# Optimization experiments

Hardware: AMD Instinct MI355X
Metric: run time of the kernel (lower is better)

The kernel has to match this reference:

```python
import jax, jax.numpy as jnp
import numpy as np

DIM = 1024
N_HEADS = 16
HEAD_DIM = DIM // N_HEADS
B, T = 2, 2048


def setup_inputs() -> dict:
    key = jax.random.key(0)
    kx, kq, kk, kv, ko = jax.random.split(key, 5)
    x = jax.random.normal(kx, (B, T, DIM), dtype=jnp.float32)
    # additive causal mask: 0 on/below diagonal, -inf above
    neg = jnp.finfo(jnp.float32).min
    causal = jnp.triu(jnp.full((T, T), neg, dtype=jnp.float32), k=1)
    mask = causal[None, None, :, :]  # [1,1,T,T]
    scale = 0.02
    Wq = jax.random.normal(kq, (DIM, DIM), dtype=jnp.float32) * scale
    Wk = jax.random.normal(kk, (DIM, DIM), dtype=jnp.float32) * scale
    Wv = jax.random.normal(kv, (DIM, DIM), dtype=jnp.float32) * scale
    Wo = jax.random.normal(ko, (DIM, DIM), dtype=jnp.float32) * scale
    return {"x": x, "mask": mask, "Wq": Wq, "Wk": Wk, "Wv": Wv, "Wo": Wo}


def reference(x, mask, Wq, Wk, Wv, Wo):
    Bs, Ts, C = x.shape
    # nn.Linear: y = x @ W.T
    q = (x @ Wq.T).reshape(Bs, Ts, N_HEADS, HEAD_DIM).transpose(0, 2, 1, 3)
    k = (x @ Wk.T).reshape(Bs, Ts, N_HEADS, HEAD_DIM).transpose(0, 2, 1, 3)
    v = (x @ Wv.T).reshape(Bs, Ts, N_HEADS, HEAD_DIM).transpose(0, 2, 1, 3)
    scores = jnp.einsum("bhqd,bhkd->bhqk", q, k) / jnp.sqrt(
        jnp.asarray(HEAD_DIM, dtype=x.dtype)
    )
    scores = scores + mask
    probs = jax.nn.softmax(scores, axis=-1)
    out = jnp.einsum("bhqk,bhkd->bhqd", probs, v)
    out = out.transpose(0, 2, 1, 3).reshape(Bs, Ts, C)
    return out @ Wo.T
```

## Files before the change

### kernel.cpp

```cpp
#include <hip/hip_runtime.h>
#include <hip/hip_bf16.h>
#include <stdint.h>

#define DIM   1024
#define NH    16
#define HD    64
#define BATCH 2
#define SEQ   2048
#define MTOK  (BATCH*SEQ)

typedef __attribute__((ext_vector_type(8))) short bf16x8;
typedef __attribute__((ext_vector_type(4))) float f32x4;
typedef __attribute__((ext_vector_type(4))) unsigned short us4;

__device__ __forceinline__ unsigned short f2bf(float f) {
  union { __hip_bfloat16 h; unsigned short u; } c;
  c.h = __float2bfloat16(f);
  return c.u;
}

__device__ __forceinline__ void gload_lds16(const unsigned short* g, unsigned short* l) {
  __builtin_amdgcn_global_load_lds(
      (const __attribute__((address_space(1))) unsigned int*)(uintptr_t)g,
      (__attribute__((address_space(3))) unsigned int*)(uintptr_t)l,
      16, 0, 0);
}

__global__ void cast_fused(const float* __restrict__ x,  const float* __restrict__ wq,
                           const float* __restrict__ wk, const float* __restrict__ wv,
                           const float* __restrict__ wo,
                           unsigned short* __restrict__ xb,
                           unsigned short* __restrict__ wqkvb,
                           unsigned short* __restrict__ wob) {
  const float* src; unsigned short* dst; int n;
  switch (blockIdx.y) {
    case 0:  src = x;  dst = xb;                n = MTOK * DIM; break;
    case 1:  src = wq; dst = wqkvb;             n = DIM * DIM;  break;
    case 2:  src = wk; dst = wqkvb +   DIM*DIM; n = DIM * DIM;  break;
    case 3:  src = wv; dst = wqkvb + 2*DIM*DIM; n = DIM * DIM;  break;
    default: src = wo; dst = wob;               n = DIM * DIM;  break;
  }
  int idx = (blockIdx.x * blockDim.x + threadIdx.x) * 4;
  const int stride = gridDim.x * blockDim.x * 4;
  for (; idx < n; idx += stride) {
    float4 v = *reinterpret_cast<const float4*>(src + idx);
    us4 o;
    o[0] = f2bf(v.x); o[1] = f2bf(v.y); o[2] = f2bf(v.z); o[3] = f2bf(v.w);
    *reinterpret_cast<us4*>(dst + idx) = o;
  }
}

template<int EPI>
__global__ __launch_bounds__(256)
void gemm_bt(const unsigned short* __restrict__ A,
             const unsigned short* __restrict__ Bw,
             int M, int N, int K, int ntn,
             unsigned short* __restrict__ Qb,
             unsigned short* __restrict__ Kb,
             unsigned short* __restrict__ Vt,
             float* __restrict__ Cf) {
  __shared__ __align__(16) unsigned short As[128 * 32];
  __shared__ __align__(16) unsigned short Bs[128 * 32];
  const int tid  = threadIdx.x;
  const int lane = tid & 63;
  const int w    = tid >> 6;
  const int wr   = w >> 1, wc = w & 1;

  const int nwg = gridDim.x;
  const int bid = blockIdx.x;
  const int swz = (nwg & 7) == 0 ? (bid & 7) * (nwg >> 3) + (bid >> 3) : bid;
  const int mt = swz / ntn, nt = swz % ntn;
  const int m0 = mt * 128, n0 = nt * 128;

  const int srow = lane >> 2;
  const int scol = (lane & 3) << 3;
  const unsigned short* Ag = A  + (size_t)(m0 + w*32 + srow) * K + scol;
  const unsigned short* Bg = Bw + (size_t)(n0 + w*32 + srow) * K + scol;
  unsigned short* AsW0 = &As[(w*32     ) * 32];
  unsigned short* AsW1 = &As[(w*32 + 16) * 32];
  unsigned short* BsW0 = &Bs[(w*32     ) * 32];
  unsigned short* BsW1 = &Bs[(w*32 + 16) * 32];

  const int l15 = lane & 15;
  const int g8  = (lane >> 4) << 3;
  f32x4 acc[4][4] = {};

  for (int k0 = 0; k0 < K; k0 += 32) {
    gload_lds16(Ag + k0,                AsW0);
    gload_lds16(Ag + (size_t)16*K + k0, AsW1);
    gload_lds16(Bg + k0,                BsW0);
    gload_lds16(Bg + (size_t)16*K + k0, BsW1);
    __syncthreads();
    bf16x8 af[4], bfr[4];
#pragma unroll
    for (int i = 0; i < 4; ++i)
      af[i] = *(const bf16x8*)&As[(wr*64 + i*16 + l15) * 32 + g8];
#pragma unroll
    for (int j = 0; j < 4; ++j)
      bfr[j] = *(const bf16x8*)&Bs[(wc*64 + j*16 + l15) * 32 + g8];
#pragma unroll
    for (int i = 0; i < 4; ++i)
#pragma unroll
      for (int j = 0; j < 4; ++j)
        acc[i][j] = __builtin_amdgcn_mfma_f32_16x16x32_bf16(af[i], bfr[j], acc[i][j], 0, 0, 0);
    __syncthreads();
  }

  const int r0 = m0 + wr*64 + ((lane >> 4) << 2);
  const int c0 = n0 + wc*64 + l15;
  if (EPI == 0) {
#pragma unroll
    for (int i = 0; i < 4; ++i) {
      const int row = r0 + i*16;
      const int bb  = row >> 11;
      const int tt  = row & (SEQ - 1);
#pragma unroll
      for (int j = 0; j < 4; ++j) {
        const int col   = c0 + j*16;
        const int which = col >> 10;
        const int hh    = (col & 1023) >> 6;
        const int dd    = col & 63;
        const int bhh   = bb * NH + hh;
        if (which == 0) {
#pragma unroll
          for (int r = 0; r < 4; ++r)
            Qb[((size_t)bhh * SEQ + tt + r) * HD + dd] = f2bf(acc[i][j][r] * 0.125f);
        } else if (which == 1) {
#pragma unroll
          for (int r = 0; r < 4; ++r)
            Kb[((size_t)bhh * SEQ + tt + r) * HD + dd] = f2bf(acc[i][j][r]);
        } else {
          us4 ov;
#pragma unroll
          for (int r = 0; r < 4; ++r) ov[r] = f2bf(acc[i][j][r]);
          *reinterpret_cast<us4*>(&Vt[((size_t)bhh * HD + dd) * SEQ + tt]) = ov;
        }
      }
    }
  } else {
#pragma unroll
    for (int i = 0; i < 4; ++i)
#pragma unroll
      for (int j = 0; j < 4; ++j)
#pragma unroll
        for (int r = 0; r < 4; ++r)
          Cf[(size_t)(r0 + i*16 + r) * N + c0 + j*16] = acc[i][j][r];
  }
}

__global__ __launch_bounds__(64)
void attn_fwd(const unsigned short* __restrict__ Qb,
              const unsigned short* __restrict__ Kb,
              const unsigned short* __restrict__ Vt,
              unsigned short* __restrict__ AO) {
  __shared__ __align__(16) unsigned short P[32 * 72];
  const int lane = threadIdx.x;
  const int l15  = lane & 15;
  const int g    = lane >> 4;
  const int g8   = g << 3;
  const int qt   = gridDim.x - 1 - blockIdx.x;
  const int q0   = qt * 32;
  const int bh   = blockIdx.y;
  const int b    = bh >> 4, h = bh & 15;

  const unsigned short* Qbh = Qb + (size_t)bh * SEQ * HD;
  const unsigned short* Kbh = Kb + (size_t)bh * SEQ * HD;
  const unsigned short* Vbh = Vt + (size_t)bh * HD * SEQ;

  bf16x8 qf[2][2];
#pragma unroll
  for (int mm = 0; mm < 2; ++mm)
#pragma unroll
    for (int dd = 0; dd < 2; ++dd)
      qf[mm][dd] = *(const bf16x8*)&Qbh[(size_t)(q0 + mm*16 + l15) * HD + dd*32 + g8];

  f32x4 o[2][4] = {};
  float mrun[8], lrun[8];
#pragma unroll
  for (int i = 0; i < 8; ++i) { mrun[i] = -1e30f; lrun[i] = 0.f; }

  const int ntile = q0 / 64 + 1;
  for (int t = 0; t < ntile; ++t) {
    const int k0 = t * 64;
    f32x4 s[2][4] = {};
#pragma unroll
    for (int dd = 0; dd < 2; ++dd) {
      bf16x8 kf[4];
#pragma unroll
      for (int nn = 0; nn < 4; ++nn)
        kf[nn] = *(const bf16x8*)&Kbh[(size_t)(k0 + nn*16 + l15) * HD + dd*32 + g8];
      __builtin_amdgcn_s_setprio(1);
#pragma unroll
      for (int mm = 0; mm < 2; ++mm)
#pragma unroll
        for (int nn = 0; nn < 4; ++nn)
          s[mm][nn] = __builtin_amdgcn_mfma_f32_16x16x32_bf16(qf[mm][dd], kf[nn], s[mm][nn], 0, 0, 0);
      __builtin_amdgcn_s_setprio(0);
    }
    if (t == ntile - 1) {
#pragma unroll
      for (int mm = 0; mm < 2; ++mm)
#pragma unroll
        for (int nn = 0; nn < 4; ++nn) {
          const int kg = k0 + nn*16 + l15;
#pragma unroll
          for (int r = 0; r < 4; ++r) {
            const int qg = q0 + mm*16 + g*4 + r;
            if (kg > qg) s[mm][nn][r] = -1e30f;
          }
        }
    }
#pragma unroll
    for (int mm = 0; mm < 2; ++mm)
#pragma unroll
      for (int r = 0; r < 4; ++r) {
        const int ri = mm*4 + r;
        float v = fmaxf(fmaxf(s[mm][0][r], s[mm][1][r]), fmaxf(s[mm][2][r], s[mm][3][r]));
        v = fmaxf(v, __shfl_xor(v, 1));
        v = fmaxf(v, __shfl_xor(v, 2));
        v = fmaxf(v, __shfl_xor(v, 4));
        v = fmaxf(v, __shfl_xor(v, 8));
        const float mnew  = fmaxf(mrun[ri], v);
        const float alpha = __expf(mrun[ri] - mnew);
        mrun[ri] = mnew;
        float rs = 0.f;
#pragma unroll
        for (int nn = 0; nn < 4; ++nn) {
          const float p = __expf(s[mm][nn][r] - mnew);
          s[mm][nn][r] = p;
          rs += p;
        }
        rs += __shfl_xor(rs, 1);
        rs += __shfl_xor(rs, 2);
        rs += __shfl_xor(rs, 4);
        rs += __shfl_xor(rs, 8);
        lrun[ri] = lrun[ri] * alpha + rs;
#pragma unroll
        for (int nn = 0; nn < 4; ++nn) o[mm][nn][r] *= alpha;
      }
#pragma unroll
    for (int mm = 0; mm < 2; ++mm)
#pragma unroll
      for (int nn = 0; nn < 4; ++nn)
#pragma unroll
        for (int r = 0; r < 4; ++r)
          P[(mm*16 + g*4 + r) * 72 + nn*16 + l15] = f2bf(s[mm][nn][r]);
    __syncthreads();
#pragma unroll
    for (int kk = 0; kk < 2; ++kk) {
      bf16x8 pa[2];
#pragma unroll
      for (int mm = 0; mm < 2; ++mm)
        pa[mm] = *(const bf16x8*)&P[(mm*16 + l15) * 72 + kk*32 + g8];
      __builtin_amdgcn_s_setprio(1);
#pragma unroll
      for (int nn = 0; nn < 4; ++nn) {
        bf16x8 vf = *(const bf16x8*)&Vbh[(size_t)(nn*16 + l15) * SEQ + k0 + kk*32 + g8];
#pragma unroll
        for (int mm = 0; mm < 2; ++mm)
          o[mm][nn] = __builtin_amdgcn_mfma_f32_16x16x32_bf16(pa[mm], vf, o[mm][nn], 0, 0, 0);
      }
      __builtin_amdgcn_s_setprio(0);
    }
    __syncthreads();
  }
#pragma unroll
  for (int mm = 0; mm < 2; ++mm)
#pragma unroll
    for (int r = 0; r < 4; ++r) {
      const float inv = 1.0f / lrun[mm*4 + r];
      const int row = b*SEQ + q0 + mm*16 + g*4 + r;
#pragma unroll
      for (int nn = 0; nn < 4; ++nn)
        AO[(size_t)row * DIM + h*HD + nn*16 + l15] = f2bf(o[mm][nn][r] * inv);
    }
}

extern "C" void kernel_launch(void* const* d_in, const int* in_sizes, int n_in,
                              void* d_out, int out_size, void* d_ws, size_t ws_size,
                              hipStream_t stream) {
  (void)in_sizes; (void)n_in; (void)out_size; (void)ws_size;
  const float* x  = (const float*)d_in[0];
  const float* Wq = (const float*)d_in[2];
  const float* Wk = (const float*)d_in[3];
  const float* Wv = (const float*)d_in[4];
  const float* Wo = (const float*)d_in[5];
  float* out = (float*)d_out;

  unsigned short* ws    = (unsigned short*)d_ws;
  unsigned short* x_bf  = ws;
  unsigned short* wqkv  = x_bf  + (size_t)MTOK * DIM;
  unsigned short* wo_bf = wqkv  + (size_t)3 * DIM * DIM;
  unsigned short* Qb    = wo_bf + (size_t)DIM * DIM;
  unsigned short* Kb    = Qb    + (size_t)MTOK * DIM;
  unsigned short* Vt    = Kb    + (size_t)MTOK * DIM;
  unsigned short* AO    = x_bf;

  cast_fused<<<dim3(1024, 5), 256, 0, stream>>>(x, Wq, Wk, Wv, Wo, x_bf, wqkv, wo_bf);

  gemm_bt<0><<<(MTOK/128) * (3*DIM/128), 256, 0, stream>>>(
      x_bf, wqkv, MTOK, 3*DIM, DIM, 3*DIM/128, Qb, Kb, Vt, nullptr);

  attn_fwd<<<dim3(SEQ/32, BATCH*NH), 64, 0, stream>>>(Qb, Kb, Vt, AO);

  gemm_bt<1><<<(MTOK/128) * (DIM/128), 256, 0, stream>>>(
      AO, wo_bf, MTOK, DIM, DIM, DIM/128, nullptr, nullptr, nullptr, out);
}
```

Baseline: 289.6 us.

## Prefetch K/V tiles into registers, lazily rescale softmax, drop block barriers

Restructures the causal attention loop so the K tiles are double-buffered in registers and the V tile for the next step is loaded right after the current PV MFMAs. This lets global loads overlap with MFMA and softmax work. Online-softmax rescaling is skipped unless some row max in the wave grows by more than 8, which removes per-tile exp and multiply work on the accumulator. The two __syncthreads around the P staging buffer are removed, relying on each wave using only its own LDS rows. The cost is much higher VGPR use from the extra fragment buffers, which could reduce occupancy.

After: 342.5 us. +18.3%, slower.

```diff
diff --git a/kernel.cpp b/kernel.cpp
--- a/kernel.cpp
+++ b/kernel.cpp
@@ -180,23 +180,37 @@
   for (int i = 0; i < 8; ++i) { mrun[i] = -1e30f; lrun[i] = 0.f; }
 
   const int ntile = q0 / 64 + 1;
-  for (int t = 0; t < ntile; ++t) {
+
+  bf16x8 ka[2][4], kb2[2][4], va[2][4];
+
+  auto issueK = [&](bf16x8 (&kf)[2][4], int k0) {
+#pragma unroll
+    for (int dd = 0; dd < 2; ++dd)
+#pragma unroll
+      for (int nn = 0; nn < 4; ++nn)
+        kf[dd][nn] = *(const bf16x8*)&Kbh[(size_t)(k0 + nn*16 + l15) * HD + dd*32 + g8];
+  };
+  auto issueV = [&](bf16x8 (&vf)[2][4], int k0) {
+#pragma unroll
+    for (int kk = 0; kk < 2; ++kk)
+#pragma unroll
+      for (int nn = 0; nn < 4; ++nn)
+        vf[kk][nn] = *(const bf16x8*)&Vbh[(size_t)(nn*16 + l15) * SEQ + k0 + kk*32 + g8];
+  };
+
+  auto tile = [&](bf16x8 (&kf)[2][4], int t) {
     const int k0 = t * 64;
     f32x4 s[2][4] = {};
-#pragma unroll
-    for (int dd = 0; dd < 2; ++dd) {
-      bf16x8 kf[4];
-#pragma unroll
-      for (int nn = 0; nn < 4; ++nn)
-        kf[nn] = *(const bf16x8*)&Kbh[(size_t)(k0 + nn*16 + l15) * HD + dd*32 + g8];
-      __builtin_amdgcn_s_setprio(1);
+    __builtin_amdgcn_s_setprio(1);
+#pragma unroll
+    for (int dd = 0; dd < 2; ++dd)
 #pragma unroll
       for (int mm = 0; mm < 2; ++mm)
 #pragma unroll
         for (int nn = 0; nn < 4; ++nn)
-          s[mm][nn] = __builtin_amdgcn_mfma_f32_16x16x32_bf16(qf[mm][dd], kf[nn], s[mm][nn], 0, 0, 0);
-      __builtin_amdgcn_s_setprio(0);
-    }
+          s[mm][nn] = __builtin_amdgcn_mfma_f32_16x16x32_bf16(qf[mm][dd], kf[dd][nn], s[mm][nn], 0, 0, 0);
+    __builtin_amdgcn_s_setprio(0);
+
     if (t == ntile - 1) {
 #pragma unroll
       for (int mm = 0; mm < 2; ++mm)
@@ -210,6 +224,8 @@
           }
         }
     }
+
+    float rmax[8], gmax = -1e30f;
 #pragma unroll
     for (int mm = 0; mm < 2; ++mm)
 #pragma unroll
@@ -220,9 +236,25 @@
         v = fmaxf(v, __shfl_xor(v, 2));
         v = fmaxf(v, __shfl_xor(v, 4));
         v = fmaxf(v, __shfl_xor(v, 8));
-        const float mnew  = fmaxf(mrun[ri], v);
-        const float alpha = __expf(mrun[ri] - mnew);
-        mrun[ri] = mnew;
+        rmax[ri] = v;
+        gmax = fmaxf(gmax, v - mrun[ri]);
+      }
+    const bool resc = __any(gmax > 8.0f);
+
+#pragma unroll
+    for (int mm = 0; mm < 2; ++mm)
+#pragma unroll
+      for (int r = 0; r < 4; ++r) {
+        const int ri = mm*4 + r;
+        float mnew = mrun[ri];
+        if (resc) {
+          mnew = fmaxf(mrun[ri], rmax[ri]);
+          const float alpha = __expf(mrun[ri] - mnew);
+          lrun[ri] *= alpha;
+#pragma unroll
+          for (int nn = 0; nn < 4; ++nn) o[mm][nn][r] *= alpha;
+          mrun[ri] = mnew;
+        }
         float rs = 0.f;
 #pragma unroll
         for (int nn = 0; nn < 4; ++nn) {
@@ -234,10 +266,9 @@
         rs += __shfl_xor(rs, 2);
         rs += __shfl_xor(rs, 4);
         rs += __shfl_xor(rs, 8);
-        lrun[ri] = lrun[ri] * alpha + rs;
-#pragma unroll
-        for (int nn = 0; nn < 4; ++nn) o[mm][nn][r] *= alpha;
+        lrun[ri] += rs;
       }
+
 #pragma unroll
     for (int mm = 0; mm < 2; ++mm)
 #pragma unroll
@@ -245,7 +276,7 @@
 #pragma unroll
         for (int r = 0; r < 4; ++r)
           P[(mm*16 + g*4 + r) * 72 + nn*16 + l15] = f2bf(s[mm][nn][r]);
-    __syncthreads();
+
 #pragma unroll
     for (int kk = 0; kk < 2; ++kk) {
       bf16x8 pa[2];
@@ -254,16 +285,26 @@
         pa[mm] = *(const bf16x8*)&P[(mm*16 + l15) * 72 + kk*32 + g8];
       __builtin_amdgcn_s_setprio(1);
 #pragma unroll
-      for (int nn = 0; nn < 4; ++nn) {
-        bf16x8 vf = *(const bf16x8*)&Vbh[(size_t)(nn*16 + l15) * SEQ + k0 + kk*32 + g8];
+      for (int nn = 0; nn < 4; ++nn)
 #pragma unroll
         for (int mm = 0; mm < 2; ++mm)
-          o[mm][nn] = __builtin_amdgcn_mfma_f32_16x16x32_bf16(pa[mm], vf, o[mm][nn], 0, 0, 0);
-      }
+          o[mm][nn] = __builtin_amdgcn_mfma_f32_16x16x32_bf16(pa[mm], va[kk][nn], o[mm][nn], 0, 0, 0);
       __builtin_amdgcn_s_setprio(0);
     }
-    __syncthreads();
-  }
+    if (t + 1 < ntile) issueV(va, k0 + 64);
+  };
+
+  issueK(ka, 0);
+  issueV(va, 0);
+  int t = 0;
+  while (t < ntile) {
+    if (t + 1 < ntile) issueK(kb2, (t + 1) * 64);
+    tile(ka, t); ++t;
+    if (t >= ntile) break;
+    if (t + 1 < ntile) issueK(ka, (t + 1) * 64);
+    tile(kb2, t); ++t;
+  }
+
 #pragma unroll
   for (int mm = 0; mm < 2; ++mm)
 #pragma unroll
```

## Shrink attention query tile to 16 rows, add lazy softmax rescale, drop barriers

Applied to the files above, without the earlier changes.

The attention kernel now handles 16 query rows per single-wave block instead of 32, doubling the grid and roughly halving registers per wave, which should raise occupancy and even out the causal work imbalance. The online-softmax rescale is skipped unless some row's max grows by more than 8 (an FA4-style lazy rescale), which saves exps and multiplies on the output accumulator. The __syncthreads around the LDS P buffer are removed because the block is a single wavefront. The costs are that each K/V tile is reloaded twice as often from L2, and the lazy rescale lets exponentials reach up to e^8, which could cost some bf16 precision in P.

After: 342.5 us. 1.18x slower.

```diff
diff --git a/kernel.cpp b/kernel.cpp
--- a/kernel.cpp
+++ b/kernel.cpp
@@ -153,13 +153,13 @@
               const unsigned short* __restrict__ Kb,
               const unsigned short* __restrict__ Vt,
               unsigned short* __restrict__ AO) {
-  __shared__ __align__(16) unsigned short P[32 * 72];
+  __shared__ __align__(16) unsigned short P[16 * 72];
   const int lane = threadIdx.x;
   const int l15  = lane & 15;
   const int g    = lane >> 4;
   const int g8   = g << 3;
   const int qt   = gridDim.x - 1 - blockIdx.x;
-  const int q0   = qt * 32;
+  const int q0   = qt * 16;
   const int bh   = blockIdx.y;
   const int b    = bh >> 4, h = bh & 15;
 
@@ -167,22 +167,20 @@
   const unsigned short* Kbh = Kb + (size_t)bh * SEQ * HD;
   const unsigned short* Vbh = Vt + (size_t)bh * HD * SEQ;
 
-  bf16x8 qf[2][2];
-#pragma unroll
-  for (int mm = 0; mm < 2; ++mm)
-#pragma unroll
-    for (int dd = 0; dd < 2; ++dd)
-      qf[mm][dd] = *(const bf16x8*)&Qbh[(size_t)(q0 + mm*16 + l15) * HD + dd*32 + g8];
-
-  f32x4 o[2][4] = {};
-  float mrun[8], lrun[8];
-#pragma unroll
-  for (int i = 0; i < 8; ++i) { mrun[i] = -1e30f; lrun[i] = 0.f; }
+  bf16x8 qf[2];
+#pragma unroll
+  for (int dd = 0; dd < 2; ++dd)
+    qf[dd] = *(const bf16x8*)&Qbh[(size_t)(q0 + l15) * HD + dd*32 + g8];
+
+  f32x4 o[4] = {};
+  float mrun[4], lrun[4];
+#pragma unroll
+  for (int i = 0; i < 4; ++i) { mrun[i] = -1e30f; lrun[i] = 0.f; }
 
   const int ntile = q0 / 64 + 1;
   for (int t = 0; t < ntile; ++t) {
     const int k0 = t * 64;
-    f32x4 s[2][4] = {};
+    f32x4 s[4] = {};
 #pragma unroll
     for (int dd = 0; dd < 2; ++dd) {
       bf16x8 kf[4];
@@ -191,89 +189,87 @@
         kf[nn] = *(const bf16x8*)&Kbh[(size_t)(k0 + nn*16 + l15) * HD + dd*32 + g8];
       __builtin_amdgcn_s_setprio(1);
 #pragma unroll
-      for (int mm = 0; mm < 2; ++mm)
-#pragma unroll
-        for (int nn = 0; nn < 4; ++nn)
-          s[mm][nn] = __builtin_amdgcn_mfma_f32_16x16x32_bf16(qf[mm][dd], kf[nn], s[mm][nn], 0, 0, 0);
+      for (int nn = 0; nn < 4; ++nn)
+        s[nn] = __builtin_amdgcn_mfma_f32_16x16x32_bf16(qf[dd], kf[nn], s[nn], 0, 0, 0);
       __builtin_amdgcn_s_setprio(0);
     }
     if (t == ntile - 1) {
 #pragma unroll
-      for (int mm = 0; mm < 2; ++mm)
-#pragma unroll
-        for (int nn = 0; nn < 4; ++nn) {
-          const int kg = k0 + nn*16 + l15;
-#pragma unroll
-          for (int r = 0; r < 4; ++r) {
-            const int qg = q0 + mm*16 + g*4 + r;
-            if (kg > qg) s[mm][nn][r] = -1e30f;
-          }
+      for (int nn = 0; nn < 4; ++nn) {
+        const int kg = k0 + nn*16 + l15;
+#pragma unroll
+        for (int r = 0; r < 4; ++r) {
+          const int qg = q0 + g*4 + r;
+          if (kg > qg) s[nn][r] = -1e30f;
         }
-    }
-#pragma unroll
-    for (int mm = 0; mm < 2; ++mm)
-#pragma unroll
-      for (int r = 0; r < 4; ++r) {
-        const int ri = mm*4 + r;
-        float v = fmaxf(fmaxf(s[mm][0][r], s[mm][1][r]), fmaxf(s[mm][2][r], s[mm][3][r]));
-        v = fmaxf(v, __shfl_xor(v, 1));
-        v = fmaxf(v, __shfl_xor(v, 2));
-        v = fmaxf(v, __shfl_xor(v, 4));
-        v = fmaxf(v, __shfl_xor(v, 8));
-        const float mnew  = fmaxf(mrun[ri], v);
-        const float alpha = __expf(mrun[ri] - mnew);
-        mrun[ri] = mnew;
-        float rs = 0.f;
-#pragma unroll
-        for (int nn = 0; nn < 4; ++nn) {
-          const float p = __expf(s[mm][nn][r] - mnew);
-          s[mm][nn][r] = p;
-          rs += p;
-        }
-        rs += __shfl_xor(rs, 1);
-        rs += __shfl_xor(rs, 2);
-        rs += __shfl_xor(rs, 4);
-        rs += __shfl_xor(rs, 8);
-        lrun[ri] = lrun[ri] * alpha + rs;
-#pragma unroll
-        for (int nn = 0; nn < 4; ++nn) o[mm][nn][r] *= alpha;
-      }
-#pragma unroll
-    for (int mm = 0; mm < 2; ++mm)
-#pragma unroll
-      for (int nn = 0; nn < 4; ++nn)
-#pragma unroll
-        for (int r = 0; r < 4; ++r)
-          P[(mm*16 + g*4 + r) * 72 + nn*16 + l15] = f2bf(s[mm][nn][r]);
-    __syncthreads();
+      }
+    }
+
+    float rmax[4], gmax = -1e30f;
+#pragma unroll
+    for (int r = 0; r < 4; ++r) {
+      float v = fmaxf(fmaxf(s[0][r], s[1][r]), fmaxf(s[2][r], s[3][r]));
+      v = fmaxf(v, __shfl_xor(v, 1));
+      v = fmaxf(v, __shfl_xor(v, 2));
+      v = fmaxf(v, __shfl_xor(v, 4));
+      v = fmaxf(v, __shfl_xor(v, 8));
+      rmax[r] = v;
+      gmax = fmaxf(gmax, v - mrun[r]);
+    }
+    const bool resc = __any(gmax > 8.0f);
+
+#pragma unroll
+    for (int r = 0; r < 4; ++r) {
+      float mnew = mrun[r];
+      if (resc) {
+        mnew = fmaxf(mrun[r], rmax[r]);
+        const float alpha = __expf(mrun[r] - mnew);
+        lrun[r] *= alpha;
+#pragma unroll
+        for (int nn = 0; nn < 4; ++nn) o[nn][r] *= alpha;
+        mrun[r] = mnew;
+      }
+      float rs = 0.f;
+#pragma unroll
+      for (int nn = 0; nn < 4; ++nn) {
+        const float p = __expf(s[nn][r] - mnew);
+        s[nn][r] = p;
+        rs += p;
+      }
+      rs += __shfl_xor(rs, 1);
+      rs += __shfl_xor(rs, 2);
+      rs += __shfl_xor(rs, 4);
+      rs += __shfl_xor(rs, 8);
+      lrun[r] += rs;
+    }
+
+#pragma unroll
+    for (int nn = 0; nn < 4; ++nn)
+#pragma unroll
+      for (int r = 0; r < 4; ++r)
+        P[(g*4 + r) * 72 + nn*16 + l15] = f2bf(s[nn][r]);
+
 #pragma unroll
     for (int kk = 0; kk < 2; ++kk) {
-      bf16x8 pa[2];
-#pragma unroll
-      for (int mm = 0; mm < 2; ++mm)
-        pa[mm] = *(const bf16x8*)&P[(mm*16 + l15) * 72 + kk*32 + g8];
+      bf16x8 pa = *(const bf16x8*)&P[l15 * 72 + kk*32 + g8];
       __builtin_amdgcn_s_setprio(1);
 #pragma unroll
       for (int nn = 0; nn < 4; ++nn) {
         bf16x8 vf = *(const bf16x8*)&Vbh[(size_t)(nn*16 + l15) * SEQ + k0 + kk*32 + g8];
-#pragma unroll
-        for (int mm = 0; mm < 2; ++mm)
-          o[mm][nn] = __builtin_amdgcn_mfma_f32_16x16x32_bf16(pa[mm], vf, o[mm][nn], 0, 0, 0);
+        o[nn] = __builtin_amdgcn_mfma_f32_16x16x32_bf16(pa, vf, o[nn], 0, 0, 0);
       }
       __builtin_amdgcn_s_setprio(0);
     }
-    __syncthreads();
-  }
-#pragma unroll
-  for (int mm = 0; mm < 2; ++mm)
-#pragma unroll
-    for (int r = 0; r < 4; ++r) {
-      const float inv = 1.0f / lrun[mm*4 + r];
-      const int row = b*SEQ + q0 + mm*16 + g*4 + r;
-#pragma unroll
-      for (int nn = 0; nn < 4; ++nn)
-        AO[(size_t)row * DIM + h*HD + nn*16 + l15] = f2bf(o[mm][nn][r] * inv);
-    }
+  }
+
+#pragma unroll
+  for (int r = 0; r < 4; ++r) {
+    const float inv = 1.0f / lrun[r];
+    const int row = b*SEQ + q0 + g*4 + r;
+#pragma unroll
+    for (int nn = 0; nn < 4; ++nn)
+      AO[(size_t)row * DIM + h*HD + nn*16 + l15] = f2bf(o[nn][r] * inv);
+  }
 }
 
 extern "C" void kernel_launch(void* const* d_in, const int* in_sizes, int n_in,
@@ -301,7 +297,7 @@
   gemm_bt<0><<<(MTOK/128) * (3*DIM/128), 256, 0, stream>>>(
       x_bf, wqkv, MTOK, 3*DIM, DIM, 3*DIM/128, Qb, Kb, Vt, nullptr);
 
-  attn_fwd<<<dim3(SEQ/32, BATCH*NH), 64, 0, stream>>>(Qb, Kb, Vt, AO);
+  attn_fwd<<<dim3(SEQ/16, BATCH*NH), 64, 0, stream>>>(Qb, Kb, Vt, AO);
 
   gemm_bt<1><<<(MTOK/128) * (DIM/128), 256, 0, stream>>>(
       AO, wo_bf, MTOK, DIM, DIM, DIM/128, nullptr, nullptr, nullptr, out);
```

## Split attention KV loop across four waves with split-K merge and lazy rescale

Applied to the files above, without the earlier changes.

The attention kernel now launches 256 threads per block, and each of its four waves handles every fourth KV tile of the same 32-row query block. Partial outputs, row maxima and row sums go to LDS, and wave 0 merges them with a log-sum-exp combine. The intent is more parallelism and shorter serial chains per block, since the causal loop length varies widely between blocks. It also adds a lazy rescale that updates the running max only when the new max exceeds it by more than 8. That saves exp and multiply work but lets unnormalized values grow by up to e^8 before rescaling. The cost is more LDS use, an extra merge stage done by a single wave, and lower occupancy from the larger shared footprint.

Result: slower. 300.7 us (+3.8%).

```diff
diff --git a/kernel.cpp b/kernel.cpp
--- a/kernel.cpp
+++ b/kernel.cpp
@@ -148,13 +148,16 @@
   }
 }
 
-__global__ __launch_bounds__(64)
+__global__ __launch_bounds__(256)
 void attn_fwd(const unsigned short* __restrict__ Qb,
               const unsigned short* __restrict__ Kb,
               const unsigned short* __restrict__ Vt,
               unsigned short* __restrict__ AO) {
-  __shared__ __align__(16) unsigned short P[32 * 72];
-  const int lane = threadIdx.x;
+  __shared__ __align__(16) float MO[4][32 * 64];
+  __shared__ float ML[4][2][32];
+  const int tid  = threadIdx.x;
+  const int lane = tid & 63;
+  const int w    = tid >> 6;
   const int l15  = lane & 15;
   const int g    = lane >> 4;
   const int g8   = g << 3;
@@ -163,6 +166,8 @@
   const int bh   = blockIdx.y;
   const int b    = bh >> 4, h = bh & 15;
 
+  unsigned short* P = reinterpret_cast<unsigned short*>(&MO[0][0]) + w * (32 * 72);
+
   const unsigned short* Qbh = Qb + (size_t)bh * SEQ * HD;
   const unsigned short* Kbh = Kb + (size_t)bh * SEQ * HD;
   const unsigned short* Vbh = Vt + (size_t)bh * HD * SEQ;
@@ -180,7 +185,7 @@
   for (int i = 0; i < 8; ++i) { mrun[i] = -1e30f; lrun[i] = 0.f; }
 
   const int ntile = q0 / 64 + 1;
-  for (int t = 0; t < ntile; ++t) {
+  for (int t = w; t < ntile; t += 4) {
     const int k0 = t * 64;
     f32x4 s[2][4] = {};
 #pragma unroll
@@ -210,6 +215,8 @@
           }
         }
     }
+
+    float rmax[8], gmax = -1e30f;
 #pragma unroll
     for (int mm = 0; mm < 2; ++mm)
 #pragma unroll
@@ -220,9 +227,25 @@
         v = fmaxf(v, __shfl_xor(v, 2));
         v = fmaxf(v, __shfl_xor(v, 4));
         v = fmaxf(v, __shfl_xor(v, 8));
-        const float mnew  = fmaxf(mrun[ri], v);
-        const float alpha = __expf(mrun[ri] - mnew);
-        mrun[ri] = mnew;
+        rmax[ri] = v;
+        gmax = fmaxf(gmax, v - mrun[ri]);
+      }
+    const bool resc = __any(gmax > 8.0f);
+
+#pragma unroll
+    for (int mm = 0; mm < 2; ++mm)
+#pragma unroll
+      for (int r = 0; r < 4; ++r) {
+        const int ri = mm*4 + r;
+        float mnew = mrun[ri];
+        if (resc) {
+          mnew = fmaxf(mrun[ri], rmax[ri]);
+          const float alpha = __expf(mrun[ri] - mnew);
+          lrun[ri] *= alpha;
+#pragma unroll
+          for (int nn = 0; nn < 4; ++nn) o[mm][nn][r] *= alpha;
+          mrun[ri] = mnew;
+        }
         float rs = 0.f;
 #pragma unroll
         for (int nn = 0; nn < 4; ++nn) {
@@ -234,10 +257,9 @@
         rs += __shfl_xor(rs, 2);
         rs += __shfl_xor(rs, 4);
         rs += __shfl_xor(rs, 8);
-        lrun[ri] = lrun[ri] * alpha + rs;
-#pragma unroll
-        for (int nn = 0; nn < 4; ++nn) o[mm][nn][r] *= alpha;
-      }
+        lrun[ri] += rs;
+      }
+
 #pragma unroll
     for (int mm = 0; mm < 2; ++mm)
 #pragma unroll
@@ -245,7 +267,7 @@
 #pragma unroll
         for (int r = 0; r < 4; ++r)
           P[(mm*16 + g*4 + r) * 72 + nn*16 + l15] = f2bf(s[mm][nn][r]);
-    __syncthreads();
+
 #pragma unroll
     for (int kk = 0; kk < 2; ++kk) {
       bf16x8 pa[2];
@@ -262,18 +284,52 @@
       }
       __builtin_amdgcn_s_setprio(0);
     }
-    __syncthreads();
-  }
+  }
+
+  __syncthreads();
 #pragma unroll
   for (int mm = 0; mm < 2; ++mm)
 #pragma unroll
-    for (int r = 0; r < 4; ++r) {
-      const float inv = 1.0f / lrun[mm*4 + r];
-      const int row = b*SEQ + q0 + mm*16 + g*4 + r;
-#pragma unroll
-      for (int nn = 0; nn < 4; ++nn)
-        AO[(size_t)row * DIM + h*HD + nn*16 + l15] = f2bf(o[mm][nn][r] * inv);
-    }
+    for (int nn = 0; nn < 4; ++nn)
+#pragma unroll
+      for (int r = 0; r < 4; ++r)
+        MO[w][(mm*16 + nn*4 + r) * 64 + lane] = o[mm][nn][r];
+  if (l15 == 0) {
+#pragma unroll
+    for (int mm = 0; mm < 2; ++mm)
+#pragma unroll
+      for (int r = 0; r < 4; ++r) {
+        ML[w][0][mm*16 + g*4 + r] = mrun[mm*4 + r];
+        ML[w][1][mm*16 + g*4 + r] = lrun[mm*4 + r];
+      }
+  }
+  __syncthreads();
+  if (w == 0) {
+#pragma unroll
+    for (int mm = 0; mm < 2; ++mm)
+#pragma unroll
+      for (int r = 0; r < 4; ++r) {
+        const int rowl = mm*16 + g*4 + r;
+        float M = fmaxf(fmaxf(ML[0][0][rowl], ML[1][0][rowl]),
+                        fmaxf(ML[2][0][rowl], ML[3][0][rowl]));
+        float fac[4], lsum = 0.f;
+#pragma unroll
+        for (int w4 = 0; w4 < 4; ++w4) {
+          fac[w4] = __expf(ML[w4][0][rowl] - M);
+          lsum += fac[w4] * ML[w4][1][rowl];
+        }
+        const float inv = 1.0f / lsum;
+        const int row = b*SEQ + q0 + rowl;
+#pragma unroll
+        for (int nn = 0; nn < 4; ++nn) {
+          float acc = 0.f;
+#pragma unroll
+          for (int w4 = 0; w4 < 4; ++w4)
+            acc += fac[w4] * MO[w4][(mm*16 + nn*4 + r) * 64 + lane];
+          AO[(size_t)row * DIM + h*HD + nn*16 + l15] = f2bf(acc * inv);
+        }
+      }
+  }
 }
 
 extern "C" void kernel_launch(void* const* d_in, const int* in_sizes, int n_in,
@@ -301,7 +357,7 @@
   gemm_bt<0><<<(MTOK/128) * (3*DIM/128), 256, 0, stream>>>(
       x_bf, wqkv, MTOK, 3*DIM, DIM, 3*DIM/128, Qb, Kb, Vt, nullptr);
 
-  attn_fwd<<<dim3(SEQ/32, BATCH*NH), 64, 0, stream>>>(Qb, Kb, Vt, AO);
+  attn_fwd<<<dim3(SEQ/32, BATCH*NH), 256, 0, stream>>>(Qb, Kb, Vt, AO);
 
   gemm_bt<1><<<(MTOK/128) * (DIM/128), 256, 0, stream>>>(
       AO, wo_bf, MTOK, DIM, DIM, DIM/128, nullptr, nullptr, nullptr, out);
```
